# Kernel optimization log

Hardware: AMD Instinct MI355X
Metric: run time of the kernel (lower is better)

Reference implementation:

```python
import jax, jax.numpy as jnp
import numpy as np

N_NODES = 100000
N_EDGES = 1600000
MAX_RADIUS = 3.0
NUM_BASIS = 3
SQRT2 = 2.0 ** 0.5
# e3nn soft_one_hot_linspace 'smooth_finite' prefactor
C_SMOOTH = 1.14136 * float(np.exp(2.0))


def _sus(x):
    # smooth unit step: exp(-1/x) for x>0 else 0 (NaN-safe for grad)
    safe = jnp.where(x > 0.0, x, 1.0)
    return jnp.where(x > 0.0, jnp.exp(-1.0 / safe), 0.0)


def radial_embed(d):
    # soft_one_hot_linspace(d, 0, max_radius, 3, basis='smooth_finite', cutoff=True) * sqrt(num_basis)
    values = jnp.linspace(0.0, MAX_RADIUS, NUM_BASIS + 2)[1:-1]  # [3]
    step = MAX_RADIUS / (NUM_BASIS + 1)
    diff = (d[:, None] - values) / step  # [E,3]
    y = C_SMOOTH * _sus(diff + 1.0) * _sus(1.0 - diff)
    return y * (NUM_BASIS ** 0.5)


def fcnet(x, w1, w2):
    # e3nn FullyConnectedNet([3,16,numel], relu): normalized weights, normalize2mom(relu)=sqrt(2)*relu
    h = SQRT2 * jax.nn.relu(x @ (w1 / w1.shape[0] ** 0.5))
    return h @ (w2 / w2.shape[0] ** 0.5)


def reference(pos, feat, edge_src, edge_dst, fc1_w1, fc1_w2, core_w1, core_w2, fc3_w1, fc3_w2, conv_w, conv_b):
    n = pos.shape[0]
    z = edge_src.shape[0] / n  # average num neighbors
    edge_vec = pos[edge_dst] - pos[edge_src]
    d = jnp.sqrt(jnp.sum(edge_vec * edge_vec, axis=1))  # edges are self-loop-free -> d > 0
    emb = radial_embed(d)  # [E,3]

    # NOTE on e3nn math: with input/mid/output parities all even and sh = 0e+1o+2e,
    # the only parity-allowed paths producing nonzero output are the 0e (scalar) paths,
    # which contract against Y_0 = 1 ('component' normalization). The 4x1e block of the
    # mid irreps is identically zero (no parity-allowed path ever populates it), so the
    # math below (scalar block only, with e3nn path weights) is exactly equivalent.
    def conv(x, w1, w2, mul_in, mul_out, path_w):
        # per-edge weights from radial MLP; keep the 0e->0e instruction block
        w = fcnet(emb, w1, w2)[:, : mul_in * mul_out].reshape(-1, mul_in, mul_out)
        msg = path_w * jnp.einsum('euw,eu->ew', w, x[edge_src])
        return jax.ops.segment_sum(msg, edge_dst, num_segments=n) / z ** 0.5

    x = conv(feat, fc1_w1, fc1_w2, 3, 4, (1.0 / 3.0) ** 0.5)  # tp1: fan_in 3*1 -> pw=1/sqrt(3)
    for i in range(3):
        x = conv(x, core_w1[i], core_w2[i], 4, 4, 0.5)  # tp2 0e path: pw=sqrt(1/4)
    x = conv(x, fc3_w1, fc3_w2, 4, 16, 0.5)  # tp3: pw=sqrt(1/4)
    # Conv1d(16, 2, 1) == pointwise linear
    return x @ conv_w.T + conv_b


def setup_inputs():
    key = jax.random.key(0)
    ks = jax.random.split(key, 12)
    pos = jax.random.uniform(ks[0], (N_NODES, 3), dtype=jnp.float32)  # unit box -> all edge lengths < max_radius
    feat = jax.random.normal(ks[1], (N_NODES, 3), dtype=jnp.float32)
    edge_src = jax.random.randint(ks[2], (N_EDGES,), 0, N_NODES, dtype=jnp.int32)
    off = jax.random.randint(ks[3], (N_EDGES,), 1, N_NODES, dtype=jnp.int32)
    edge_dst = ((edge_src + off) % N_NODES).astype(jnp.int32)  # radius_graph has no self-loops
    return {
        'pos': pos,
        'feat': feat,
        'edge_src': edge_src,
        'edge_dst': edge_dst,
        'fc1_w1': jax.random.normal(ks[4], (3, 16), jnp.float32),
        'fc1_w2': jax.random.normal(ks[5], (16, 12), jnp.float32),
        'core_w1': jax.random.normal(ks[6], (3, 3, 16), jnp.float32),
        'core_w2': jax.random.normal(ks[7], (3, 16, 48), jnp.float32),
        'fc3_w1': jax.random.normal(ks[8], (3, 16), jnp.float32),
        'fc3_w2': jax.random.normal(ks[9], (16, 64), jnp.float32),
        'conv_w': jax.random.normal(ks[10], (2, 16), jnp.float32) * 0.25,
        'conv_b': jax.random.normal(ks[11], (2,), jnp.float32) * 0.1,
    }
```

## Files before the change

### kernel.cpp

```cpp
#include <hip/hip_runtime.h>


#define BCAP 4608
#define NBMAX 400

__device__ __forceinline__ float sus_f(float x) {
    return x > 0.0f ? __expf(-1.0f / x) : 0.0f;
}

__global__ __launch_bounds__(128) void k_prep_g(
    const float* __restrict__ w2, const float* __restrict__ cw,
    float* __restrict__ gbuf)
{
    int idx = threadIdx.x;
    int k = idx >> 3, u = (idx >> 1) & 3, c = idx & 1;
    float s = 0.0f;
    #pragma unroll
    for (int w = 0; w < 16; ++w)
        s = fmaf(w2[k * 64 + u * 16 + w], cw[c * 16 + w], s);
    gbuf[idx] = s;
}

__global__ __launch_bounds__(256) void k_bin(
    const int* __restrict__ src, const int* __restrict__ dst,
    int* __restrict__ gcur, int* __restrict__ ptmp,
    int nedges, int nb)
{
    __shared__ int cnt[NBMAX];
    __shared__ int gb[NBMAX];
    for (int b = threadIdx.x; b < nb; b += 256) cnt[b] = 0;
    __syncthreads();

    int base = blockIdx.x * 2048 + threadIdx.x * 8;
    int pk[8]; int bk[8]; short r[8];
    int ss[8], dd[8];
    if (base + 7 < nedges) {
        int4 s0 = *(const int4*)&src[base];
        int4 s1 = *(const int4*)&src[base + 4];
        int4 d0 = *(const int4*)&dst[base];
        int4 d1 = *(const int4*)&dst[base + 4];
        ss[0]=s0.x; ss[1]=s0.y; ss[2]=s0.z; ss[3]=s0.w;
        ss[4]=s1.x; ss[5]=s1.y; ss[6]=s1.z; ss[7]=s1.w;
        dd[0]=d0.x; dd[1]=d0.y; dd[2]=d0.z; dd[3]=d0.w;
        dd[4]=d1.x; dd[5]=d1.y; dd[6]=d1.z; dd[7]=d1.w;
        #pragma unroll
        for (int i = 0; i < 8; ++i) {
            int b = dd[i] >> 8;
            bk[i] = b;
            pk[i] = (ss[i] << 8) | (dd[i] & 255);
            r[i] = (short)atomicAdd(&cnt[b], 1);
        }
    } else {
        #pragma unroll
        for (int i = 0; i < 8; ++i) {
            int e = base + i;
            if (e < nedges) {
                int s = src[e], t = dst[e];
                int b = t >> 8;
                bk[i] = b;
                pk[i] = (s << 8) | (t & 255);
                r[i] = (short)atomicAdd(&cnt[b], 1);
            } else bk[i] = -1;
        }
    }
    __syncthreads();
    for (int b = threadIdx.x; b < nb; b += 256) {
        int c = cnt[b];
        gb[b] = c > 0 ? atomicAdd(&gcur[b], c) : 0;
    }
    __syncthreads();
    #pragma unroll
    for (int i = 0; i < 8; ++i) {
        if (bk[i] >= 0) {
            int p = gb[bk[i]] + (int)r[i];
            if (p < BCAP)
                ptmp[bk[i] * BCAP + p] = pk[i];
        }
    }
}

__global__ __launch_bounds__(256) void k_build(
    const int* __restrict__ gcur, const int* __restrict__ ptmp,
    int* __restrict__ pidx, int2* __restrict__ offs2,
    int n, int nb)
{
    int b = blockIdx.x;
    int cnt = gcur[b]; if (cnt > BCAP) cnt = BCAP;

    __shared__ int stage[BCAP];
    __shared__ int perm[BCAP];
    __shared__ int deg[256];
    __shared__ int loffs[256];
    __shared__ int cur[256];

    const int* tin = ptmp + b * BCAP;
    for (int j = threadIdx.x; j < cnt; j += 256) stage[j] = tin[j];
    deg[threadIdx.x] = 0;
    __syncthreads();

    for (int j = threadIdx.x; j < cnt; j += 256)
        atomicAdd(&deg[stage[j] & 255], 1);
    __syncthreads();

    {
        int t = threadIdx.x;
        int v = deg[t];
        loffs[t] = v; __syncthreads();
        for (int off = 1; off < 256; off <<= 1) {
            int val = (t >= off) ? loffs[t - off] : 0;
            __syncthreads();
            loffs[t] += val;
            __syncthreads();
        }
        int incl = loffs[t];
        __syncthreads();
        loffs[t] = incl - v;
        cur[t] = incl - v;
        __syncthreads();
    }

    {
        int nid0 = b << 8;
        int nn = n - nid0; if (nn > 256) nn = 256;
        int t = threadIdx.x;
        if (t < nn) {
            int st = b * BCAP + loffs[t];
            offs2[nid0 + t] = make_int2(st, st + deg[t]);
        }
    }

    for (int j = threadIdx.x; j < cnt; j += 256) {
        int pkd = stage[j];
        perm[atomicAdd(&cur[pkd & 255], 1)] = pkd;
    }
    __syncthreads();

    int* tout = pidx + b * BCAP;
    for (int j = threadIdx.x; j < cnt; j += 256) tout[j] = perm[j];
}

__global__ __launch_bounds__(256) void k_emb(
    const float* __restrict__ pos, const int* __restrict__ gcur,
    const int* __restrict__ pidx, float4* __restrict__ ebuf)
{
    int b = blockIdx.y;
    int j = blockIdx.x * 256 + threadIdx.x;
    if (j >= gcur[b]) return;
    int pkd = pidx[b * BCAP + j];
    int s = pkd >> 8;
    int t = (b << 8) | (pkd & 255);
    float dx = pos[3 * t + 0] - pos[3 * s + 0];
    float dy = pos[3 * t + 1] - pos[3 * s + 1];
    float dz = pos[3 * t + 2] - pos[3 * s + 2];
    float d = sqrtf(dx * dx + dy * dy + dz * dz);
    const float C = 1.14136f * 7.3890560989306495f;
    float e0, e1, e2;
    { float f = (d - 0.75f) * (1.0f / 0.75f);
      e0 = C * sus_f(f + 1.0f) * sus_f(1.0f - f); }
    { float f = (d - 1.50f) * (1.0f / 0.75f);
      e1 = C * sus_f(f + 1.0f) * sus_f(1.0f - f); }
    { float f = (d - 2.25f) * (1.0f / 0.75f);
      e2 = C * sus_f(f + 1.0f) * sus_f(1.0f - f); }
    ebuf[(size_t)b * BCAP + j] = make_float4(__int_as_float(s), e0, e1, e2);
}


__global__ __launch_bounds__(256) void k_node_l1(
    const float* __restrict__ feat, const float4* __restrict__ edata,
    const int2* __restrict__ offs2,
    const float* __restrict__ w1, const float* __restrict__ w2,
    float* __restrict__ xout, int n)
{
    __shared__ float lw[16 * 20];
    if (threadIdx.x < 192) {
        int k = threadIdx.x / 12, r = threadIdx.x % 12;
        lw[k * 20 + r] = w2[k * 12 + r];
    }
    __syncthreads();

    int g = blockIdx.x * 256 + threadIdx.x;
    int nd = g >> 2;
    if (nd >= n) return;
    int t = g & 3;

    float w1r[3][4];
    #pragma unroll
    for (int j = 0; j < 3; ++j)
        #pragma unroll
        for (int kk = 0; kk < 4; ++kk) w1r[j][kk] = w1[j * 16 + 4 * t + kk];

    float O[4][3];
    #pragma unroll
    for (int kk = 0; kk < 4; ++kk)
        #pragma unroll
        for (int u = 0; u < 3; ++u) O[kk][u] = 0.0f;

    int2 se = offs2[nd];
    int e = se.x;
    for (; e + 4 <= se.y; e += 4) {
        float4 ed0 = edata[e], ed1 = edata[e + 1],
               ed2 = edata[e + 2], ed3 = edata[e + 3];
        int s0 = __float_as_int(ed0.x), s1 = __float_as_int(ed1.x),
            s2 = __float_as_int(ed2.x), s3 = __float_as_int(ed3.x);
        float f00 = feat[3*s0], f01 = feat[3*s0+1], f02 = feat[3*s0+2];
        float f10 = feat[3*s1], f11 = feat[3*s1+1], f12 = feat[3*s1+2];
        float f20 = feat[3*s2], f21 = feat[3*s2+1], f22 = feat[3*s2+2];
        float f30 = feat[3*s3], f31 = feat[3*s3+1], f32 = feat[3*s3+2];
        #pragma unroll
        for (int kk = 0; kk < 4; ++kk) {
            float a, h;
            a = fmaf(ed0.y, w1r[0][kk], fmaf(ed0.z, w1r[1][kk], ed0.w * w1r[2][kk]));
            h = a > 0.0f ? a : 0.0f;
            O[kk][0] = fmaf(h, f00, O[kk][0]); O[kk][1] = fmaf(h, f01, O[kk][1]); O[kk][2] = fmaf(h, f02, O[kk][2]);
            a = fmaf(ed1.y, w1r[0][kk], fmaf(ed1.z, w1r[1][kk], ed1.w * w1r[2][kk]));
            h = a > 0.0f ? a : 0.0f;
            O[kk][0] = fmaf(h, f10, O[kk][0]); O[kk][1] = fmaf(h, f11, O[kk][1]); O[kk][2] = fmaf(h, f12, O[kk][2]);
            a = fmaf(ed2.y, w1r[0][kk], fmaf(ed2.z, w1r[1][kk], ed2.w * w1r[2][kk]));
            h = a > 0.0f ? a : 0.0f;
            O[kk][0] = fmaf(h, f20, O[kk][0]); O[kk][1] = fmaf(h, f21, O[kk][1]); O[kk][2] = fmaf(h, f22, O[kk][2]);
            a = fmaf(ed3.y, w1r[0][kk], fmaf(ed3.z, w1r[1][kk], ed3.w * w1r[2][kk]));
            h = a > 0.0f ? a : 0.0f;
            O[kk][0] = fmaf(h, f30, O[kk][0]); O[kk][1] = fmaf(h, f31, O[kk][1]); O[kk][2] = fmaf(h, f32, O[kk][2]);
        }
    }
    for (; e < se.y; ++e) {
        float4 ed = edata[e];
        int s = __float_as_int(ed.x);
        float f0 = feat[3*s], f1 = feat[3*s+1], f2 = feat[3*s+2];
        #pragma unroll
        for (int kk = 0; kk < 4; ++kk) {
            float a = fmaf(ed.y, w1r[0][kk], fmaf(ed.z, w1r[1][kk], ed.w * w1r[2][kk]));
            float h = a > 0.0f ? a : 0.0f;
            O[kk][0] = fmaf(h, f0, O[kk][0]);
            O[kk][1] = fmaf(h, f1, O[kk][1]);
            O[kk][2] = fmaf(h, f2, O[kk][2]);
        }
    }

    float p0 = 0.f, p1 = 0.f, p2 = 0.f, p3 = 0.f;
    #pragma unroll
    for (int kk = 0; kk < 4; ++kk)
        #pragma unroll
        for (int u = 0; u < 3; ++u) {
            const float4 q = *(const float4*)&lw[(4 * t + kk) * 20 + u * 4];
            float o = O[kk][u];
            p0 = fmaf(o, q.x, p0); p1 = fmaf(o, q.y, p1);
            p2 = fmaf(o, q.z, p2); p3 = fmaf(o, q.w, p3);
        }
    p0 += __shfl_xor(p0, 1); p1 += __shfl_xor(p1, 1);
    p2 += __shfl_xor(p2, 1); p3 += __shfl_xor(p3, 1);
    p0 += __shfl_xor(p0, 2); p1 += __shfl_xor(p1, 2);
    p2 += __shfl_xor(p2, 2); p3 += __shfl_xor(p3, 2);
    if (t == 0) {
        const float S = 0.051031036307982884f;
        float4 o; o.x = p0 * S; o.y = p1 * S; o.z = p2 * S; o.w = p3 * S;
        ((float4*)xout)[nd] = o;
    }
}

__global__ __launch_bounds__(256) void k_node_core(
    const float4* __restrict__ xin, const float4* __restrict__ edata,
    const int2* __restrict__ offs2,
    const float* __restrict__ w1, const float* __restrict__ w2,
    float* __restrict__ xout, int n)
{
    __shared__ float lw[16 * 20];
    {
        int idx = threadIdx.x;
        int k = idx >> 4, r = idx & 15;
        lw[k * 20 + r] = w2[k * 48 + r];
    }
    __syncthreads();

    int g = blockIdx.x * 256 + threadIdx.x;
    int nd = g >> 2;
    if (nd >= n) return;
    int t = g & 3;

    float w1r[3][4];
    #pragma unroll
    for (int j = 0; j < 3; ++j)
        #pragma unroll
        for (int kk = 0; kk < 4; ++kk) w1r[j][kk] = w1[j * 16 + 4 * t + kk];

    float O[4][4];
    #pragma unroll
    for (int kk = 0; kk < 4; ++kk)
        #pragma unroll
        for (int u = 0; u < 4; ++u) O[kk][u] = 0.0f;

    int2 se = offs2[nd];
    int e = se.x;
    for (; e + 4 <= se.y; e += 4) {
        float4 ed0 = edata[e], ed1 = edata[e + 1],
               ed2 = edata[e + 2], ed3 = edata[e + 3];
        float4 x0 = xin[__float_as_int(ed0.x)];
        float4 x1 = xin[__float_as_int(ed1.x)];
        float4 x2 = xin[__float_as_int(ed2.x)];
        float4 x3 = xin[__float_as_int(ed3.x)];
        #pragma unroll
        for (int kk = 0; kk < 4; ++kk) {
            float a, h;
            a = fmaf(ed0.y, w1r[0][kk], fmaf(ed0.z, w1r[1][kk], ed0.w * w1r[2][kk]));
            h = a > 0.0f ? a : 0.0f;
            O[kk][0] = fmaf(h, x0.x, O[kk][0]); O[kk][1] = fmaf(h, x0.y, O[kk][1]);
            O[kk][2] = fmaf(h, x0.z, O[kk][2]); O[kk][3] = fmaf(h, x0.w, O[kk][3]);
            a = fmaf(ed1.y, w1r[0][kk], fmaf(ed1.z, w1r[1][kk], ed1.w * w1r[2][kk]));
            h = a > 0.0f ? a : 0.0f;
            O[kk][0] = fmaf(h, x1.x, O[kk][0]); O[kk][1] = fmaf(h, x1.y, O[kk][1]);
            O[kk][2] = fmaf(h, x1.z, O[kk][2]); O[kk][3] = fmaf(h, x1.w, O[kk][3]);
            a = fmaf(ed2.y, w1r[0][kk], fmaf(ed2.z, w1r[1][kk], ed2.w * w1r[2][kk]));
            h = a > 0.0f ? a : 0.0f;
            O[kk][0] = fmaf(h, x2.x, O[kk][0]); O[kk][1] = fmaf(h, x2.y, O[kk][1]);
            O[kk][2] = fmaf(h, x2.z, O[kk][2]); O[kk][3] = fmaf(h, x2.w, O[kk][3]);
            a = fmaf(ed3.y, w1r[0][kk], fmaf(ed3.z, w1r[1][kk], ed3.w * w1r[2][kk]));
            h = a > 0.0f ? a : 0.0f;
            O[kk][0] = fmaf(h, x3.x, O[kk][0]); O[kk][1] = fmaf(h, x3.y, O[kk][1]);
            O[kk][2] = fmaf(h, x3.z, O[kk][2]); O[kk][3] = fmaf(h, x3.w, O[kk][3]);
        }
    }
    for (; e < se.y; ++e) {
        float4 ed = edata[e];
        float4 x = xin[__float_as_int(ed.x)];
        #pragma unroll
        for (int kk = 0; kk < 4; ++kk) {
            float a = fmaf(ed.y, w1r[0][kk], fmaf(ed.z, w1r[1][kk], ed.w * w1r[2][kk]));
            float h = a > 0.0f ? a : 0.0f;
            O[kk][0] = fmaf(h, x.x, O[kk][0]); O[kk][1] = fmaf(h, x.y, O[kk][1]);
            O[kk][2] = fmaf(h, x.z, O[kk][2]); O[kk][3] = fmaf(h, x.w, O[kk][3]);
        }
    }

    float p0 = 0.f, p1 = 0.f, p2 = 0.f, p3 = 0.f;
    #pragma unroll
    for (int kk = 0; kk < 4; ++kk)
        #pragma unroll
        for (int u = 0; u < 4; ++u) {
            const float4 q = *(const float4*)&lw[(4 * t + kk) * 20 + u * 4];
            float o = O[kk][u];
            p0 = fmaf(o, q.x, p0); p1 = fmaf(o, q.y, p1);
            p2 = fmaf(o, q.z, p2); p3 = fmaf(o, q.w, p3);
        }
    p0 += __shfl_xor(p0, 1); p1 += __shfl_xor(p1, 1);
    p2 += __shfl_xor(p2, 1); p3 += __shfl_xor(p3, 1);
    p0 += __shfl_xor(p0, 2); p1 += __shfl_xor(p1, 2);
    p2 += __shfl_xor(p2, 2); p3 += __shfl_xor(p3, 2);
    if (t == 0) {
        const float S = 0.04419417382415922f;
        float4 o; o.x = p0 * S; o.y = p1 * S; o.z = p2 * S; o.w = p3 * S;
        ((float4*)xout)[nd] = o;
    }
}

__global__ __launch_bounds__(256) void k_node_fc3_final(
    const float4* __restrict__ xin, const float4* __restrict__ edata,
    const int2* __restrict__ offs2,
    const float* __restrict__ w1, const float* __restrict__ gbuf,
    const float* __restrict__ cb,
    float* __restrict__ out, int n)
{
    __shared__ float lg[128];
    if (threadIdx.x < 128) lg[threadIdx.x] = gbuf[threadIdx.x];
    __syncthreads();

    int g = blockIdx.x * 256 + threadIdx.x;
    int nd = g >> 2;
    if (nd >= n) return;
    int t = g & 3;

    float w1r[3][4];
    #pragma unroll
    for (int j = 0; j < 3; ++j)
        #pragma unroll
        for (int kk = 0; kk < 4; ++kk) w1r[j][kk] = w1[j * 16 + 4 * t + kk];

    float O[4][4];
    #pragma unroll
    for (int kk = 0; kk < 4; ++kk)
        #pragma unroll
        for (int u = 0; u < 4; ++u) O[kk][u] = 0.0f;

    int2 se = offs2[nd];
    int e = se.x;
    for (; e + 4 <= se.y; e += 4) {
        float4 ed0 = edata[e], ed1 = edata[e + 1],
               ed2 = edata[e + 2], ed3 = edata[e + 3];
        float4 x0 = xin[__float_as_int(ed0.x)];
        float4 x1 = xin[__float_as_int(ed1.x)];
        float4 x2 = xin[__float_as_int(ed2.x)];
        float4 x3 = xin[__float_as_int(ed3.x)];
        #pragma unroll
        for (int kk = 0; kk < 4; ++kk) {
            float a, h;
            a = fmaf(ed0.y, w1r[0][kk], fmaf(ed0.z, w1r[1][kk], ed0.w * w1r[2][kk]));
            h = a > 0.0f ? a : 0.0f;
            O[kk][0] = fmaf(h, x0.x, O[kk][0]); O[kk][1] = fmaf(h, x0.y, O[kk][1]);
            O[kk][2] = fmaf(h, x0.z, O[kk][2]); O[kk][3] = fmaf(h, x0.w, O[kk][3]);
            a = fmaf(ed1.y, w1r[0][kk], fmaf(ed1.z, w1r[1][kk], ed1.w * w1r[2][kk]));
            h = a > 0.0f ? a : 0.0f;
            O[kk][0] = fmaf(h, x1.x, O[kk][0]); O[kk][1] = fmaf(h, x1.y, O[kk][1]);
            O[kk][2] = fmaf(h, x1.z, O[kk][2]); O[kk][3] = fmaf(h, x1.w, O[kk][3]);
            a = fmaf(ed2.y, w1r[0][kk], fmaf(ed2.z, w1r[1][kk], ed2.w * w1r[2][kk]));
            h = a > 0.0f ? a : 0.0f;
            O[kk][0] = fmaf(h, x2.x, O[kk][0]); O[kk][1] = fmaf(h, x2.y, O[kk][1]);
            O[kk][2] = fmaf(h, x2.z, O[kk][2]); O[kk][3] = fmaf(h, x2.w, O[kk][3]);
            a = fmaf(ed3.y, w1r[0][kk], fmaf(ed3.z, w1r[1][kk], ed3.w * w1r[2][kk]));
            h = a > 0.0f ? a : 0.0f;
            O[kk][0] = fmaf(h, x3.x, O[kk][0]); O[kk][1] = fmaf(h, x3.y, O[kk][1]);
            O[kk][2] = fmaf(h, x3.z, O[kk][2]); O[kk][3] = fmaf(h, x3.w, O[kk][3]);
        }
    }
    for (; e < se.y; ++e) {
        float4 ed = edata[e];
        float4 x = xin[__float_as_int(ed.x)];
        #pragma unroll
        for (int kk = 0; kk < 4; ++kk) {
            float a = fmaf(ed.y, w1r[0][kk], fmaf(ed.z, w1r[1][kk], ed.w * w1r[2][kk]));
            float h = a > 0.0f ? a : 0.0f;
            O[kk][0] = fmaf(h, x.x, O[kk][0]); O[kk][1] = fmaf(h, x.y, O[kk][1]);
            O[kk][2] = fmaf(h, x.z, O[kk][2]); O[kk][3] = fmaf(h, x.w, O[kk][3]);
        }
    }

    float a0 = 0.f, a1 = 0.f;
    #pragma unroll
    for (int kk = 0; kk < 4; ++kk)
        #pragma unroll
        for (int u = 0; u < 4; ++u) {
            float o = O[kk][u];
            const float2 q = *(const float2*)&lg[(((4 * t + kk) * 4) + u) * 2];
            a0 = fmaf(o, q.x, a0);
            a1 = fmaf(o, q.y, a1);
        }
    a0 += __shfl_xor(a0, 1); a1 += __shfl_xor(a1, 1);
    a0 += __shfl_xor(a0, 2); a1 += __shfl_xor(a1, 2);
    if (t == 0) {
        const float S = 0.04419417382415922f;
        float2 o; o.x = fmaf(a0, S, cb[0]); o.y = fmaf(a1, S, cb[1]);
        ((float2*)out)[nd] = o;
    }
}


extern "C" void kernel_launch(void* const* d_in, const int* in_sizes, int n_in,
                              void* d_out, int out_size, void* d_ws, size_t ws_size,
                              hipStream_t stream) {
    const float* pos     = (const float*)d_in[0];
    const float* feat    = (const float*)d_in[1];
    const int*   esrc    = (const int*)d_in[2];
    const int*   edst    = (const int*)d_in[3];
    const float* fc1_w1  = (const float*)d_in[4];
    const float* fc1_w2  = (const float*)d_in[5];
    const float* core_w1 = (const float*)d_in[6];
    const float* core_w2 = (const float*)d_in[7];
    const float* fc3_w1  = (const float*)d_in[8];
    const float* fc3_w2  = (const float*)d_in[9];
    const float* conv_w  = (const float*)d_in[10];
    const float* conv_b  = (const float*)d_in[11];
    float* out = (float*)d_out;

    const int E = in_sizes[2];
    const int N = in_sizes[0] / 3;
    const int nb = (N + 255) >> 8;

    float4* ebuf = (float4*)d_ws;
    int* ptmp  = (int*)(ebuf + (size_t)nb * BCAP);
    int* pidx  = ptmp + (size_t)nb * BCAP;
    float* xa  = (float*)(pidx + (size_t)nb * BCAP);
    float* xb  = xa + (size_t)4 * N;
    int2* offs2 = (int2*)(xb + (size_t)4 * N);
    int* gcur  = (int*)(offs2 + N);
    float* gbuf = (float*)(gcur + ((nb + 3) & ~3));

    int g4 = (4 * N + 255) / 256;

    hipMemsetAsync(gcur, 0, (size_t)nb * sizeof(int), stream);
    k_prep_g<<<1, 128, 0, stream>>>(fc3_w2, conv_w, gbuf);
    k_bin<<<(E + 2047) / 2048, 256, 0, stream>>>(esrc, edst, gcur, ptmp, E, nb);
    k_build<<<nb, 256, 0, stream>>>(gcur, ptmp, pidx, offs2, N, nb);
    {
        dim3 eg(BCAP / 256, nb);
        k_emb<<<eg, 256, 0, stream>>>(pos, gcur, pidx, ebuf);
    }

    k_node_l1<<<g4, 256, 0, stream>>>(feat, ebuf, offs2, fc1_w1, fc1_w2, xa, N);
    k_node_core<<<g4, 256, 0, stream>>>((const float4*)xa, ebuf, offs2,
                                        core_w1 + 0, core_w2 + 0, xb, N);
    k_node_core<<<g4, 256, 0, stream>>>((const float4*)xb, ebuf, offs2,
                                        core_w1 + 48, core_w2 + 768, xa, N);
    k_node_core<<<g4, 256, 0, stream>>>((const float4*)xa, ebuf, offs2,
                                        core_w1 + 96, core_w2 + 1536, xb, N);
    k_node_fc3_final<<<g4, 256, 0, stream>>>((const float4*)xb, ebuf, offs2,
                                             fc3_w1, gbuf, conv_b, out, N);
}
```

Measured before the change: 243.3 us.

## Sort nodes by in-degree so wavefronts process similar-degree nodes together

Builds a degree histogram in k_build, prefix-scans it, and scatters node ids into a degree-sorted order array. The five node kernels then map each 4-lane group to order[q] instead of the node id, so nodes in the same wavefront have similar edge counts and less lane divergence in the edge loops. In exchange it adds two small kernels, an extra indirection, and writes to xout with less coalescing, because the sorted order scatters the output rows.

```diff
diff --git a/kernel.cpp b/kernel.cpp
--- a/kernel.cpp
+++ b/kernel.cpp
@@ -82,6 +82,7 @@
 __global__ __launch_bounds__(256) void k_build(
     const int* __restrict__ gcur, const int* __restrict__ ptmp,
     int* __restrict__ pidx, int2* __restrict__ offs2,
+    int* __restrict__ dhist,
     int n, int nb)
 {
     int b = blockIdx.x;
@@ -126,6 +127,8 @@
         if (t < nn) {
             int st = b * BCAP + loffs[t];
             offs2[nid0 + t] = make_int2(st, st + deg[t]);
+            int dg = deg[t]; if (dg > 255) dg = 255;
+            atomicAdd(&dhist[dg], 1);
         }
     }
 
@@ -137,6 +140,33 @@
 
     int* tout = pidx + b * BCAP;
     for (int j = threadIdx.x; j < cnt; j += 256) tout[j] = perm[j];
+}
+
+__global__ __launch_bounds__(256) void k_dscan(const int* __restrict__ dhist,
+                                               int* __restrict__ dcur) {
+    __shared__ int ls[256];
+    int t = threadIdx.x;
+    int v = dhist[t];
+    ls[t] = v; __syncthreads();
+    for (int off = 1; off < 256; off <<= 1) {
+        int val = (t >= off) ? ls[t - off] : 0;
+        __syncthreads();
+        ls[t] += val;
+        __syncthreads();
+    }
+    dcur[t] = ls[t] - v;
+}
+
+__global__ __launch_bounds__(256) void k_dscatter(
+    const int2* __restrict__ offs2, int* __restrict__ dcur,
+    int* __restrict__ order, int n)
+{
+    int nd = blockIdx.x * 256 + threadIdx.x;
+    if (nd >= n) return;
+    int2 se = offs2[nd];
+    int dg = se.y - se.x; if (dg > 255) dg = 255;
+    int p = atomicAdd(&dcur[dg], 1);
+    order[p] = nd;
 }
 
 __global__ __launch_bounds__(256) void k_emb(
@@ -167,7 +197,7 @@
 
 __global__ __launch_bounds__(256) void k_node_l1(
     const float* __restrict__ feat, const float4* __restrict__ edata,
-    const int2* __restrict__ offs2,
+    const int2* __restrict__ offs2, const int* __restrict__ order,
     const float* __restrict__ w1, const float* __restrict__ w2,
     float* __restrict__ xout, int n)
 {
@@ -179,8 +209,9 @@
     __syncthreads();
 
     int g = blockIdx.x * 256 + threadIdx.x;
-    int nd = g >> 2;
-    if (nd >= n) return;
+    int q = g >> 2;
+    if (q >= n) return;
+    int nd = order[q];
     int t = g & 3;
 
     float w1r[3][4];
@@ -242,10 +273,10 @@
     for (int kk = 0; kk < 4; ++kk)
         #pragma unroll
         for (int u = 0; u < 3; ++u) {
-            const float4 q = *(const float4*)&lw[(4 * t + kk) * 20 + u * 4];
+            const float4 qv = *(const float4*)&lw[(4 * t + kk) * 20 + u * 4];
             float o = O[kk][u];
-            p0 = fmaf(o, q.x, p0); p1 = fmaf(o, q.y, p1);
-            p2 = fmaf(o, q.z, p2); p3 = fmaf(o, q.w, p3);
+            p0 = fmaf(o, qv.x, p0); p1 = fmaf(o, qv.y, p1);
+            p2 = fmaf(o, qv.z, p2); p3 = fmaf(o, qv.w, p3);
         }
     p0 += __shfl_xor(p0, 1); p1 += __shfl_xor(p1, 1);
     p2 += __shfl_xor(p2, 1); p3 += __shfl_xor(p3, 1);
@@ -260,7 +291,7 @@
 
 __global__ __launch_bounds__(256) void k_node_core(
     const float4* __restrict__ xin, const float4* __restrict__ edata,
-    const int2* __restrict__ offs2,
+    const int2* __restrict__ offs2, const int* __restrict__ order,
     const float* __restrict__ w1, const float* __restrict__ w2,
     float* __restrict__ xout, int n)
 {
@@ -273,8 +304,9 @@
     __syncthreads();
 
     int g = blockIdx.x * 256 + threadIdx.x;
-    int nd = g >> 2;
-    if (nd >= n) return;
+    int q = g >> 2;
+    if (q >= n) return;
+    int nd = order[q];
     int t = g & 3;
 
     float w1r[3][4];
@@ -336,10 +368,10 @@
     for (int kk = 0; kk < 4; ++kk)
         #pragma unroll
         for (int u = 0; u < 4; ++u) {
-            const float4 q = *(const float4*)&lw[(4 * t + kk) * 20 + u * 4];
+            const float4 qv = *(const float4*)&lw[(4 * t + kk) * 20 + u * 4];
             float o = O[kk][u];
-            p0 = fmaf(o, q.x, p0); p1 = fmaf(o, q.y, p1);
-            p2 = fmaf(o, q.z, p2); p3 = fmaf(o, q.w, p3);
+            p0 = fmaf(o, qv.x, p0); p1 = fmaf(o, qv.y, p1);
+            p2 = fmaf(o, qv.z, p2); p3 = fmaf(o, qv.w, p3);
         }
     p0 += __shfl_xor(p0, 1); p1 += __shfl_xor(p1, 1);
     p2 += __shfl_xor(p2, 1); p3 += __shfl_xor(p3, 1);
@@ -354,7 +386,7 @@
 
 __global__ __launch_bounds__(256) void k_node_fc3_final(
     const float4* __restrict__ xin, const float4* __restrict__ edata,
-    const int2* __restrict__ offs2,
+    const int2* __restrict__ offs2, const int* __restrict__ order,
     const float* __restrict__ w1, const float* __restrict__ gbuf,
     const float* __restrict__ cb,
     float* __restrict__ out, int n)
@@ -364,8 +396,9 @@
     __syncthreads();
 
     int g = blockIdx.x * 256 + threadIdx.x;
-    int nd = g >> 2;
-    if (nd >= n) return;
+    int q = g >> 2;
+    if (q >= n) return;
+    int nd = order[q];
     int t = g & 3;
 
     float w1r[3][4];
@@ -428,9 +461,9 @@
         #pragma unroll
         for (int u = 0; u < 4; ++u) {
             float o = O[kk][u];
-            const float2 q = *(const float2*)&lg[(((4 * t + kk) * 4) + u) * 2];
-            a0 = fmaf(o, q.x, a0);
-            a1 = fmaf(o, q.y, a1);
+            const float2 qv = *(const float2*)&lg[(((4 * t + kk) * 4) + u) * 2];
+            a0 = fmaf(o, qv.x, a0);
+            a1 = fmaf(o, qv.y, a1);
         }
     a0 += __shfl_xor(a0, 1); a1 += __shfl_xor(a1, 1);
     a0 += __shfl_xor(a0, 2); a1 += __shfl_xor(a1, 2);
@@ -469,27 +502,34 @@
     float* xa  = (float*)(pidx + (size_t)nb * BCAP);
     float* xb  = xa + (size_t)4 * N;
     int2* offs2 = (int2*)(xb + (size_t)4 * N);
-    int* gcur  = (int*)(offs2 + N);
-    float* gbuf = (float*)(gcur + ((nb + 3) & ~3));
+    int* order = (int*)(offs2 + N);
+    int* gcur  = order + N;
+    int* dhist = gcur + nb;
+    int* dcur  = dhist + 256;
+    float* gbuf = (float*)(dcur + 256);
 
     int g4 = (4 * N + 255) / 256;
-
-    hipMemsetAsync(gcur, 0, (size_t)nb * sizeof(int), stream);
+    int ngrid = (N + 255) / 256;
+
+    hipMemsetAsync(gcur, 0, (size_t)(nb + 256) * sizeof(int), stream);
     k_prep_g<<<1, 128, 0, stream>>>(fc3_w2, conv_w, gbuf);
     k_bin<<<(E + 2047) / 2048, 256, 0, stream>>>(esrc, edst, gcur, ptmp, E, nb);
-    k_build<<<nb, 256, 0, stream>>>(gcur, ptmp, pidx, offs2, N, nb);
+    k_build<<<nb, 256, 0, stream>>>(gcur, ptmp, pidx, offs2, dhist, N, nb);
+    k_dscan<<<1, 256, 0, stream>>>(dhist, dcur);
+    k_dscatter<<<ngrid, 256, 0, stream>>>(offs2, dcur, order, N);
     {
         dim3 eg(BCAP / 256, nb);
         k_emb<<<eg, 256, 0, stream>>>(pos, gcur, pidx, ebuf);
     }
 
-    k_node_l1<<<g4, 256, 0, stream>>>(feat, ebuf, offs2, fc1_w1, fc1_w2, xa, N);
-    k_node_core<<<g4, 256, 0, stream>>>((const float4*)xa, ebuf, offs2,
+    k_node_l1<<<g4, 256, 0, stream>>>(feat, ebuf, offs2, order,
+                                      fc1_w1, fc1_w2, xa, N);
+    k_node_core<<<g4, 256, 0, stream>>>((const float4*)xa, ebuf, offs2, order,
                                         core_w1 + 0, core_w2 + 0, xb, N);
-    k_node_core<<<g4, 256, 0, stream>>>((const float4*)xb, ebuf, offs2,
+    k_node_core<<<g4, 256, 0, stream>>>((const float4*)xb, ebuf, offs2, order,
                                         core_w1 + 48, core_w2 + 768, xa, N);
-    k_node_core<<<g4, 256, 0, stream>>>((const float4*)xa, ebuf, offs2,
+    k_node_core<<<g4, 256, 0, stream>>>((const float4*)xa, ebuf, offs2, order,
                                         core_w1 + 96, core_w2 + 1536, xb, N);
-    k_node_fc3_final<<<g4, 256, 0, stream>>>((const float4*)xb, ebuf, offs2,
+    k_node_fc3_final<<<g4, 256, 0, stream>>>((const float4*)xb, ebuf, offs2, order,
                                              fc3_w1, gbuf, conv_b, out, N);
 }
```

Result: slower. 820.7 us (+237.3%).
